# Performance work log

Hardware: AMD Instinct MI355X
Metric: run time of the kernel (lower is better)

## Reference

```python
import jax, jax.numpy as jnp
import numpy as np

D = 1024      # d_model
H = 16        # num_heads
DH = D // H   # head_dim = 64
BASE = 10000.0


def setup_inputs() -> dict:
    key = jax.random.key(0)
    ks = jax.random.split(key, 5)
    lengths = np.array([1024, 768, 896, 1024], dtype=np.int32)
    cu = np.concatenate([[0], np.cumsum(lengths)]).astype(np.int32)
    T = int(cu[-1])  # 3712 packed tokens
    x = jax.random.normal(ks[0], (T, D), dtype=jnp.float32)
    Wqkv = jax.random.normal(ks[1], (D, 3 * D), dtype=jnp.float32) / np.sqrt(D)
    bqkv = jax.random.normal(ks[2], (3 * D,), dtype=jnp.float32) * 0.02
    Wo = jax.random.normal(ks[3], (D, D), dtype=jnp.float32) / np.sqrt(D)
    bo = jax.random.normal(ks[4], (D,), dtype=jnp.float32) * 0.02
    return {"x": x, "Wqkv": Wqkv, "bqkv": bqkv, "Wo": Wo, "bo": bo,
            "cu_seqlens": jnp.asarray(cu), "max_seqlen": 1024}


def reference(x, Wqkv, bqkv, Wo, bo, cu_seqlens, max_seqlen):
    T = x.shape[0]
    B = cu_seqlens.shape[0] - 1
    S = int(max_seqlen)

    # fused qkv projection: [T, 3, H, DH]
    qkv = (x @ Wqkv + bqkv).reshape(T, 3, H, DH)
    q, k, v = qkv[:, 0], qkv[:, 1], qkv[:, 2]

    # per-token sequence id and within-sequence position (RoPE resets per seq)
    tok = jnp.arange(T)
    seq_id = jnp.searchsorted(cu_seqlens, tok, side='right') - 1  # [T]
    pos = tok - cu_seqlens[seq_id]                                # [T]

    # RoPE, non-interleaved (rotate-half over full head_dim)
    inv_freq = 1.0 / (BASE ** (jnp.arange(0, DH, 2, dtype=jnp.float32) / DH))
    ang = pos[:, None].astype(jnp.float32) * inv_freq             # [T, DH/2]
    cos = jnp.cos(ang)[:, None, :]                                # [T, 1, DH/2]
    sin = jnp.sin(ang)[:, None, :]

    def rope(t):
        t1, t2 = t[..., : DH // 2], t[..., DH // 2:]
        return jnp.concatenate([t1 * cos - t2 * sin, t2 * cos + t1 * sin], axis=-1)

    q, k = rope(q), rope(k)

    # scatter packed tokens into padded [B, S, H, DH] (varlen attention)
    qp = jnp.zeros((B, S, H, DH), x.dtype).at[seq_id, pos].set(q)
    kp = jnp.zeros((B, S, H, DH), x.dtype).at[seq_id, pos].set(k)
    vp = jnp.zeros((B, S, H, DH), x.dtype).at[seq_id, pos].set(v)
    valid = jnp.zeros((B, S), bool).at[seq_id, pos].set(True)

    scale = 1.0 / np.sqrt(DH)
    scores = jnp.einsum('bqhd,bkhd->bhqk', qp, kp) * scale        # [B,H,S,S]
    causal = jnp.tril(jnp.ones((S, S), bool))
    mask = causal[None, None] & valid[:, None, None, :]
    scores = jnp.where(mask, scores, jnp.asarray(-1e30, scores.dtype))
    attn = jax.nn.softmax(scores, axis=-1)
    op = jnp.einsum('bhqk,bkhd->bqhd', attn, vp)                  # [B,S,H,DH]

    # unpad back to packed layout, then output projection (W_o)
    out = op[seq_id, pos].reshape(T, D)
    return out @ Wo + bo
```

## Files before the change

kernel.cpp:

```cpp
#include <hip/hip_runtime.h>

typedef _Float16 f16;
typedef _Float16 f16x8 __attribute__((ext_vector_type(8)));
typedef _Float16 f16x4 __attribute__((ext_vector_type(4)));
typedef float f32x4 __attribute__((ext_vector_type(4)));

#define MFMA16(a, b, c) __builtin_amdgcn_mfma_f32_16x16x32_f16((a), (b), (c), 0, 0, 0)

typedef __attribute__((address_space(3))) void lds_void;
typedef const __attribute__((address_space(1))) void g_void;
__device__ __forceinline__ void async_copy16(void* lds, const void* g) {
    __builtin_amdgcn_global_load_lds((g_void*)g, (lds_void*)lds, 16, 0, 0);
}

__global__ void cvt_x(const float* __restrict__ in, f16* __restrict__ out, int n) {
    int i4 = (blockIdx.x * 256 + threadIdx.x) * 4;
    if (i4 >= n) return;
    float4 v = *reinterpret_cast<const float4*>(in + i4);
    f16x4 o;
    o[0] = (f16)v.x; o[1] = (f16)v.y; o[2] = (f16)v.z; o[3] = (f16)v.w;
    *reinterpret_cast<f16x4*>(out + i4) = o;
}

__global__ void wtrans(const float* __restrict__ in, f16* __restrict__ out, int K, int N) {
    __shared__ f16 tile[64][65];
    int n0 = blockIdx.x * 64, k0 = blockIdx.y * 64;
    int c = threadIdx.x & 63, rb = threadIdx.x >> 6;
#pragma unroll
    for (int it = 0; it < 16; ++it) {
        int r = rb + it * 4;
        tile[r][c] = (f16)in[(size_t)(k0 + r) * N + n0 + c];
    }
    __syncthreads();
#pragma unroll
    for (int it = 0; it < 16; ++it) {
        int rr = rb + it * 4;
        out[(size_t)(n0 + rr) * K + k0 + c] = tile[c][rr];
    }
}

#define BM 128
#define BN 128
#define BKK 32
__global__ __launch_bounds__(256) void gemm_tile(
    const f16* __restrict__ A, const f16* __restrict__ Bt,
    const float* __restrict__ bias, f16* __restrict__ Ch, float* __restrict__ Cf,
    int M, int N, int K) {
    __shared__ f16 lA[2][BM * BKK];
    __shared__ f16 lB[2][BN * BKK];
    int tid = threadIdx.x;
    int lane = tid & 63, w = tid >> 6;
    int lr = lane & 15, lg = lane >> 4;
    int wm = (w & 1) * 64, wn = (w >> 1) * 64;
    int bx = blockIdx.x, by = blockIdx.y;

    int srow = tid >> 2;
    int scol = (tid & 3) * 8;
    const f16* ga0 = A  + (size_t)min(by * BM + srow,      M - 1) * K + scol;
    const f16* ga1 = A  + (size_t)min(by * BM + 64 + srow, M - 1) * K + scol;
    const f16* gb0 = Bt + (size_t)min(bx * BN + srow,      N - 1) * K + scol;
    const f16* gb1 = Bt + (size_t)min(bx * BN + 64 + srow, N - 1) * K + scol;

    f32x4 acc[4][4] = {};
    int NT = K / BKK;

#define STAGE(curb, kt) do {                                        \
        int ko = (kt) * BKK;                                        \
        async_copy16(&lA[curb][w * 512],        ga0 + ko);          \
        async_copy16(&lA[curb][2048 + w * 512], ga1 + ko);          \
        async_copy16(&lB[curb][w * 512],        gb0 + ko);          \
        async_copy16(&lB[curb][2048 + w * 512], gb1 + ko);          \
    } while (0)

    STAGE(0, 0);
    __syncthreads();
    int cur = 0;
    for (int kt = 0; kt < NT; ++kt) {
        if (kt + 1 < NT) STAGE(cur ^ 1, kt + 1);
        f16x8 af[4], bf[4];
#pragma unroll
        for (int i = 0; i < 4; ++i) {
            af[i] = *reinterpret_cast<const f16x8*>(&lA[cur][(wm + i * 16 + lr) * BKK + lg * 8]);
            bf[i] = *reinterpret_cast<const f16x8*>(&lB[cur][(wn + i * 16 + lr) * BKK + lg * 8]);
        }
#pragma unroll
        for (int mi = 0; mi < 4; ++mi)
#pragma unroll
            for (int ni = 0; ni < 4; ++ni)
                acc[mi][ni] = MFMA16(af[mi], bf[ni], acc[mi][ni]);
        __syncthreads();
        cur ^= 1;
    }
#undef STAGE

#pragma unroll
    for (int mi = 0; mi < 4; ++mi) {
#pragma unroll
        for (int ni = 0; ni < 4; ++ni) {
            int col = bx * BN + wn + ni * 16 + lr;
            float bv = bias ? bias[col] : 0.f;
#pragma unroll
            for (int r = 0; r < 4; ++r) {
                int row = by * BM + wm + mi * 16 + 4 * lg + r;
                if (row >= M) continue;
                float v = acc[mi][ni][r] + bv;
                if (Ch) Ch[(size_t)row * N + col] = (f16)v;
                else    Cf[(size_t)row * N + col] = v;
            }
        }
    }
}

__global__ void rope_qk(const f16* __restrict__ qkv, const int* __restrict__ cu,
                        int Bn, int T, int Spad,
                        f16* __restrict__ qh2, f16* __restrict__ kh2) {
    int idx = blockIdx.x * 256 + threadIdx.x;
    if (idx >= T * 512) return;
    int i = idx & 31;
    int hh = (idx >> 5) & 15;
    int t = idx >> 9;
    int b = 0, pos = t;
    for (int q = 0; q < Bn; ++q) {
        int lo = cu[q], hi = cu[q + 1];
        if (t >= lo && t < hi) { b = q; pos = t - lo; break; }
    }
    float inv = exp2f((float)i * (-13.287712379549449f / 32.f));
    float ang = (float)pos * inv;
    float sn, cs;
    __sincosf(ang, &sn, &cs);
    size_t base = (size_t)t * 3072 + hh * 64 + i;
    float q1 = (float)qkv[base],        q2 = (float)qkv[base + 32];
    float k1 = (float)qkv[base + 1024], k2 = (float)qkv[base + 1056];
    size_t ob = ((size_t)(b * 16 + hh) * Spad + pos) * 64 + i;
    qh2[ob]      = (f16)(q1 * cs - q2 * sn);
    qh2[ob + 32] = (f16)(q2 * cs + q1 * sn);
    kh2[ob]      = (f16)(k1 * cs - k2 * sn);
    kh2[ob + 32] = (f16)(k2 * cs + k1 * sn);
}

__global__ void v_trans(const f16* __restrict__ qkv, const int* __restrict__ cu,
                        int Bn, int T, int Spad, f16* __restrict__ vt) {
    __shared__ f16 tile[64][65];
    int h = blockIdx.y;
    int t0 = blockIdx.x * 64;
    int c = threadIdx.x & 63, rb = threadIdx.x >> 6;
#pragma unroll
    for (int it = 0; it < 16; ++it) {
        int r = rb + it * 4;
        int t = t0 + r;
        f16 v = (f16)0.f;
        if (t < T) v = qkv[(size_t)t * 3072 + 2048 + h * 64 + c];
        tile[r][c] = v;
    }
    __syncthreads();
    int t = t0 + c;
    int bb = 0, pos = -1;
    if (t < T) {
        for (int q = 0; q < Bn; ++q) {
            int lo = cu[q], hi = cu[q + 1];
            if (t >= lo && t < hi) { bb = q; pos = t - lo; }
        }
    }
#pragma unroll
    for (int it = 0; it < 16; ++it) {
        int d = rb + it * 4;
        if (pos >= 0) vt[((size_t)(bb * 16 + h) * 64 + d) * Spad + pos] = tile[c][d];
    }
}

__global__ __launch_bounds__(64) void attn_fwd(
    const f16* __restrict__ qh2, const f16* __restrict__ kh2,
    const f16* __restrict__ vt, const int* __restrict__ cu,
    f16* __restrict__ oh, int Spad, int nq, int Bn) {
    int wgid = blockIdx.x;
    int nbh = Bn * 16;
    int b, h, qi;
    if ((nbh & 7) == 0) {
        int xcd = wgid & 7, rest = wgid >> 3, nbh8 = nbh >> 3;
        int bhhi = rest % nbh8;
        qi = (nq - 1) - rest / nbh8;
        int bhv = (bhhi << 3) | xcd;
        b = bhv >> 4; h = bhv & 15;
    } else {
        qi = wgid % nq;
        int bhv = wgid / nq;
        b = bhv >> 4; h = bhv & 15;
    }
    int bh = b * 16 + h;
    int s0 = cu[b];
    int len = cu[b + 1] - s0;
    int q0 = qi * 32;
    if (q0 >= len) return;
    int lane = threadIdx.x & 63, lr = lane & 15, lg = lane >> 4;
    __shared__ f16 pl[2][16][40];

    const f16* qbase = qh2 + (size_t)bh * Spad * 64;
    const f16* kbase = kh2 + (size_t)bh * Spad * 64;
    const f16* vbase = vt  + (size_t)bh * 64 * Spad;

    f16x8 qf[2][2];
#pragma unroll
    for (int qt = 0; qt < 2; ++qt) {
        const f16* qp = qbase + (size_t)(q0 + 16 * qt + lr) * 64 + 8 * lg;
        qf[qt][0] = *reinterpret_cast<const f16x8*>(qp);
        qf[qt][1] = *reinterpret_cast<const f16x8*>(qp + 32);
    }
    float mrun[2] = {-1e30f, -1e30f}, lrun[2] = {0.f, 0.f};
    f32x4 oacc[2][4] = {};

    int kend = min(q0 + 32, len);
    for (int kk0 = 0; kk0 < kend; kk0 += 32) {
        f16x8 kf[2][2];
#pragma unroll
        for (int j = 0; j < 2; ++j) {
            const f16* kp = kbase + (size_t)(kk0 + 16 * j + lr) * 64 + 8 * lg;
            kf[j][0] = *reinterpret_cast<const f16x8*>(kp);
            kf[j][1] = *reinterpret_cast<const f16x8*>(kp + 32);
        }
        f32x4 st[2][2];
#pragma unroll
        for (int qt = 0; qt < 2; ++qt)
#pragma unroll
            for (int j = 0; j < 2; ++j) {
                f32x4 z = {0, 0, 0, 0};
                z = MFMA16(kf[j][0], qf[qt][0], z);
                z = MFMA16(kf[j][1], qf[qt][1], z);
                st[qt][j] = z;
            }
#pragma unroll
        for (int qt = 0; qt < 2; ++qt) {
            int qr = q0 + 16 * qt + lr;
            float sv[2][4];
            float mx = -1e30f;
#pragma unroll
            for (int j = 0; j < 2; ++j)
#pragma unroll
                for (int r = 0; r < 4; ++r) {
                    int kc = kk0 + 16 * j + 4 * lg + r;
                    float v = st[qt][j][r] * 0.125f;
                    if (kc > qr || kc >= len) v = -1e30f;
                    sv[j][r] = v;
                    mx = fmaxf(mx, v);
                }
            mx = fmaxf(mx, __shfl_xor(mx, 16, 64));
            mx = fmaxf(mx, __shfl_xor(mx, 32, 64));
            float mnew = fmaxf(mrun[qt], mx);
            float al = __expf(mrun[qt] - mnew);
            mrun[qt] = mnew;
            float rs = 0.f;
            f16x4 pk0, pk1;
#pragma unroll
            for (int r = 0; r < 4; ++r) {
                float p0 = __expf(sv[0][r] - mnew);
                float p1 = __expf(sv[1][r] - mnew);
                rs += p0 + p1;
                pk0[r] = (f16)p0;
                pk1[r] = (f16)p1;
            }
            rs += __shfl_xor(rs, 16, 64);
            rs += __shfl_xor(rs, 32, 64);
            lrun[qt] = lrun[qt] * al + rs;
            *reinterpret_cast<f16x4*>(&pl[qt][lr][4 * lg])      = pk0;
            *reinterpret_cast<f16x4*>(&pl[qt][lr][16 + 4 * lg]) = pk1;
#pragma unroll
            for (int dt = 0; dt < 4; ++dt)
#pragma unroll
                for (int r = 0; r < 4; ++r) oacc[qt][dt][r] *= al;
        }
        __syncthreads();
        f16x8 pa0 = *reinterpret_cast<const f16x8*>(&pl[0][lr][8 * lg]);
        f16x8 pa1 = *reinterpret_cast<const f16x8*>(&pl[1][lr][8 * lg]);
#pragma unroll
        for (int dt = 0; dt < 4; ++dt) {
            f16x8 vf = *reinterpret_cast<const f16x8*>(vbase + (size_t)(16 * dt + lr) * Spad + kk0 + 8 * lg);
            oacc[0][dt] = MFMA16(vf, pa0, oacc[0][dt]);
            oacc[1][dt] = MFMA16(vf, pa1, oacc[1][dt]);
        }
        __syncthreads();
    }
#pragma unroll
    for (int qt = 0; qt < 2; ++qt) {
        int qr = q0 + 16 * qt + lr;
        if (qr >= len) continue;
        float linv = 1.f / lrun[qt];
        f16* orow = oh + (size_t)(s0 + qr) * 1024 + h * 64;
#pragma unroll
        for (int dt = 0; dt < 4; ++dt) {
            f16x4 ov;
#pragma unroll
            for (int r = 0; r < 4; ++r) ov[r] = (f16)(oacc[qt][dt][r] * linv);
            *reinterpret_cast<f16x4*>(orow + 16 * dt + 4 * lg) = ov;
        }
    }
}

extern "C" void kernel_launch(void* const* d_in, const int* in_sizes, int n_in,
                              void* d_out, int out_size, void* d_ws, size_t ws_size,
                              hipStream_t stream) {
    const float* x    = (const float*)d_in[0];
    const float* Wqkv = (const float*)d_in[1];
    const float* bqkv = (const float*)d_in[2];
    const float* Wo   = (const float*)d_in[3];
    const float* bo   = (const float*)d_in[4];
    const int*   cu   = (const int*)d_in[5];

    const int Dm = 1024;
    int T  = in_sizes[0] / Dm;
    int Bn = in_sizes[5] - 1;
    int Spad = 1024;

    auto al = [](size_t v) { return (v + 255) & ~(size_t)255; };
    char* w = (char*)d_ws;
    size_t off = 0;
    f16* xh     = (f16*)(w + off); off = al(off + (size_t)2 * T * 1024);
    f16* qkvh   = (f16*)(w + off); off = al(off + (size_t)2 * T * 3072);
    f16* wqkvT  = (f16*)(w + off); off = al(off + (size_t)2 * 3072 * 1024);
    f16* woT    = (f16*)(w + off); off = al(off + (size_t)2 * 1024 * 1024);
    f16* qh2    = (f16*)(w + off); off = al(off + (size_t)2 * Bn * 16 * 64 * (size_t)Spad);
    f16* kh2    = (f16*)(w + off); off = al(off + (size_t)2 * Bn * 16 * 64 * (size_t)Spad);
    f16* vtp    = (f16*)(w + off); off = al(off + (size_t)2 * Bn * 16 * 64 * (size_t)Spad);
    f16* ohp    = (f16*)(w + off); off = al(off + (size_t)2 * T * 1024);
    (void)ws_size;

    {
        int n = T * 1024;
        cvt_x<<<(n / 4 + 255) / 256, 256, 0, stream>>>(x, xh, n);
    }
    wtrans<<<dim3(3072 / 64, 1024 / 64), 256, 0, stream>>>(Wqkv, wqkvT, 1024, 3072);
    wtrans<<<dim3(1024 / 64, 1024 / 64), 256, 0, stream>>>(Wo, woT, 1024, 1024);
    {
        dim3 g(3072 / BN, (T + BM - 1) / BM);
        gemm_tile<<<g, 256, 0, stream>>>(xh, wqkvT, bqkv, qkvh, nullptr, T, 3072, 1024);
    }
    {
        int total = T * 512;
        rope_qk<<<(total + 255) / 256, 256, 0, stream>>>(qkvh, cu, Bn, T, Spad, qh2, kh2);
    }
    v_trans<<<dim3((T + 63) / 64, 16), 256, 0, stream>>>(qkvh, cu, Bn, T, Spad, vtp);
    {
        int nq = Spad / 32;
        int ngrid = nq * 16 * Bn;
        attn_fwd<<<ngrid, 64, 0, stream>>>(qh2, kh2, vtp, cu, ohp, Spad, nq, Bn);
    }
    {
        dim3 g(1024 / BN, (T + BM - 1) / BM);
        gemm_tile<<<g, 256, 0, stream>>>(ohp, woT, bo, nullptr, (float*)d_out, T, 1024, 1024);
    }
}
```

Before: 149.0 us.

## Widen attention query tile, prefetch K, prescale Q, remap GEMM tiles across XCDs

The attention kernel now processes 64 query rows per single-wave workgroup instead of 32, so each K/V tile loaded is reused across four 16-row query tiles. The next K tile is register-prefetched during softmax. The 1/sqrt(d) scale moves into the RoPE kernel's Q write, removing a multiply per score. The GEMM switches to a 1D grid with an XCD-aware tile remap to improve L2 locality. Costs include higher register pressure and fewer attention workgroups, plus extra causal-masked work at the diagonal with the larger tile.

```diff
diff --git a/kernel.cpp b/kernel.cpp
--- a/kernel.cpp
+++ b/kernel.cpp
@@ -45,14 +45,17 @@
 __global__ __launch_bounds__(256) void gemm_tile(
     const f16* __restrict__ A, const f16* __restrict__ Bt,
     const float* __restrict__ bias, f16* __restrict__ Ch, float* __restrict__ Cf,
-    int M, int N, int K) {
+    int M, int N, int K, int nbx) {
     __shared__ f16 lA[2][BM * BKK];
     __shared__ f16 lB[2][BN * BKK];
     int tid = threadIdx.x;
     int lane = tid & 63, w = tid >> 6;
     int lr = lane & 15, lg = lane >> 4;
     int wm = (w & 1) * 64, wn = (w >> 1) * 64;
-    int bx = blockIdx.x, by = blockIdx.y;
+
+    int nwg = gridDim.x, wg = blockIdx.x;
+    int tile = ((nwg & 7) == 0) ? ((wg & 7) * (nwg >> 3) + (wg >> 3)) : wg;
+    int by = tile / nbx, bx = tile % nbx;
 
     int srow = tid >> 2;
     int scol = (tid & 3) * 8;
@@ -132,8 +135,8 @@
     float q1 = (float)qkv[base],        q2 = (float)qkv[base + 32];
     float k1 = (float)qkv[base + 1024], k2 = (float)qkv[base + 1056];
     size_t ob = ((size_t)(b * 16 + hh) * Spad + pos) * 64 + i;
-    qh2[ob]      = (f16)(q1 * cs - q2 * sn);
-    qh2[ob + 32] = (f16)(q2 * cs + q1 * sn);
+    qh2[ob]      = (f16)((q1 * cs - q2 * sn) * 0.125f);
+    qh2[ob + 32] = (f16)((q2 * cs + q1 * sn) * 0.125f);
     kh2[ob]      = (f16)(k1 * cs - k2 * sn);
     kh2[ob + 32] = (f16)(k2 * cs + k1 * sn);
 }
@@ -189,37 +192,42 @@
     int bh = b * 16 + h;
     int s0 = cu[b];
     int len = cu[b + 1] - s0;
-    int q0 = qi * 32;
+    int q0 = qi * 64;
     if (q0 >= len) return;
     int lane = threadIdx.x & 63, lr = lane & 15, lg = lane >> 4;
-    __shared__ f16 pl[2][16][40];
+    __shared__ f16 pl[4][16][40];
 
     const f16* qbase = qh2 + (size_t)bh * Spad * 64;
     const f16* kbase = kh2 + (size_t)bh * Spad * 64;
     const f16* vbase = vt  + (size_t)bh * 64 * Spad;
 
-    f16x8 qf[2][2];
-#pragma unroll
-    for (int qt = 0; qt < 2; ++qt) {
+    f16x8 qf[4][2];
+#pragma unroll
+    for (int qt = 0; qt < 4; ++qt) {
         const f16* qp = qbase + (size_t)(q0 + 16 * qt + lr) * 64 + 8 * lg;
         qf[qt][0] = *reinterpret_cast<const f16x8*>(qp);
         qf[qt][1] = *reinterpret_cast<const f16x8*>(qp + 32);
     }
-    float mrun[2] = {-1e30f, -1e30f}, lrun[2] = {0.f, 0.f};
-    f32x4 oacc[2][4] = {};
-
-    int kend = min(q0 + 32, len);
-    for (int kk0 = 0; kk0 < kend; kk0 += 32) {
-        f16x8 kf[2][2];
-#pragma unroll
-        for (int j = 0; j < 2; ++j) {
-            const f16* kp = kbase + (size_t)(kk0 + 16 * j + lr) * 64 + 8 * lg;
-            kf[j][0] = *reinterpret_cast<const f16x8*>(kp);
-            kf[j][1] = *reinterpret_cast<const f16x8*>(kp + 32);
-        }
-        f32x4 st[2][2];
-#pragma unroll
-        for (int qt = 0; qt < 2; ++qt)
+    float mrun[4] = {-1e30f, -1e30f, -1e30f, -1e30f};
+    float lrun[4] = {0.f, 0.f, 0.f, 0.f};
+    f32x4 oacc[4][4] = {};
+
+    int kend = min(q0 + 64, len);
+    int ntk = (kend + 31) >> 5;
+
+    f16x8 kf[2][2], kn[2][2];
+#pragma unroll
+    for (int j = 0; j < 2; ++j) {
+        const f16* kp = kbase + (size_t)(16 * j + lr) * 64 + 8 * lg;
+        kf[j][0] = *reinterpret_cast<const f16x8*>(kp);
+        kf[j][1] = *reinterpret_cast<const f16x8*>(kp + 32);
+    }
+
+    for (int kt = 0; kt < ntk; ++kt) {
+        int kk0 = kt << 5;
+        f32x4 st[4][2];
+#pragma unroll
+        for (int qt = 0; qt < 4; ++qt)
 #pragma unroll
             for (int j = 0; j < 2; ++j) {
                 f32x4 z = {0, 0, 0, 0};
@@ -227,8 +235,16 @@
                 z = MFMA16(kf[j][1], qf[qt][1], z);
                 st[qt][j] = z;
             }
-#pragma unroll
-        for (int qt = 0; qt < 2; ++qt) {
+        if (kt + 1 < ntk) {
+#pragma unroll
+            for (int j = 0; j < 2; ++j) {
+                const f16* kp = kbase + (size_t)(kk0 + 32 + 16 * j + lr) * 64 + 8 * lg;
+                kn[j][0] = *reinterpret_cast<const f16x8*>(kp);
+                kn[j][1] = *reinterpret_cast<const f16x8*>(kp + 32);
+            }
+        }
+#pragma unroll
+        for (int qt = 0; qt < 4; ++qt) {
             int qr = q0 + 16 * qt + lr;
             float sv[2][4];
             float mx = -1e30f;
@@ -237,7 +253,7 @@
 #pragma unroll
                 for (int r = 0; r < 4; ++r) {
                     int kc = kk0 + 16 * j + 4 * lg + r;
-                    float v = st[qt][j][r] * 0.125f;
+                    float v = st[qt][j][r];
                     if (kc > qr || kc >= len) v = -1e30f;
                     sv[j][r] = v;
                     mx = fmaxf(mx, v);
@@ -268,18 +284,26 @@
                 for (int r = 0; r < 4; ++r) oacc[qt][dt][r] *= al;
         }
         __syncthreads();
-        f16x8 pa0 = *reinterpret_cast<const f16x8*>(&pl[0][lr][8 * lg]);
-        f16x8 pa1 = *reinterpret_cast<const f16x8*>(&pl[1][lr][8 * lg]);
+        f16x8 pa[4];
+#pragma unroll
+        for (int qt = 0; qt < 4; ++qt)
+            pa[qt] = *reinterpret_cast<const f16x8*>(&pl[qt][lr][8 * lg]);
 #pragma unroll
         for (int dt = 0; dt < 4; ++dt) {
             f16x8 vf = *reinterpret_cast<const f16x8*>(vbase + (size_t)(16 * dt + lr) * Spad + kk0 + 8 * lg);
-            oacc[0][dt] = MFMA16(vf, pa0, oacc[0][dt]);
-            oacc[1][dt] = MFMA16(vf, pa1, oacc[1][dt]);
+#pragma unroll
+            for (int qt = 0; qt < 4; ++qt)
+                oacc[qt][dt] = MFMA16(vf, pa[qt], oacc[qt][dt]);
         }
         __syncthreads();
-    }
-#pragma unroll
-    for (int qt = 0; qt < 2; ++qt) {
+#pragma unroll
+        for (int j = 0; j < 2; ++j) {
+            kf[j][0] = kn[j][0];
+            kf[j][1] = kn[j][1];
+        }
+    }
+#pragma unroll
+    for (int qt = 0; qt < 4; ++qt) {
         int qr = q0 + 16 * qt + lr;
         if (qr >= len) continue;
         float linv = 1.f / lrun[qt];
@@ -329,8 +353,8 @@
     wtrans<<<dim3(3072 / 64, 1024 / 64), 256, 0, stream>>>(Wqkv, wqkvT, 1024, 3072);
     wtrans<<<dim3(1024 / 64, 1024 / 64), 256, 0, stream>>>(Wo, woT, 1024, 1024);
     {
-        dim3 g(3072 / BN, (T + BM - 1) / BM);
-        gemm_tile<<<g, 256, 0, stream>>>(xh, wqkvT, bqkv, qkvh, nullptr, T, 3072, 1024);
+        int nbx = 3072 / BN, nby = (T + BM - 1) / BM;
+        gemm_tile<<<nbx * nby, 256, 0, stream>>>(xh, wqkvT, bqkv, qkvh, nullptr, T, 3072, 1024, nbx);
     }
     {
         int total = T * 512;
@@ -338,12 +362,12 @@
     }
     v_trans<<<dim3((T + 63) / 64, 16), 256, 0, stream>>>(qkvh, cu, Bn, T, Spad, vtp);
     {
-        int nq = Spad / 32;
+        int nq = Spad / 64;
         int ngrid = nq * 16 * Bn;
         attn_fwd<<<ngrid, 64, 0, stream>>>(qh2, kh2, vtp, cu, ohp, Spad, nq, Bn);
     }
     {
-        dim3 g(1024 / BN, (T + BM - 1) / BM);
-        gemm_tile<<<g, 256, 0, stream>>>(ohp, woT, bo, nullptr, (float*)d_out, T, 1024, 1024);
-    }
-}
+        int nbx = 1024 / BN, nby = (T + BM - 1) / BM;
+        gemm_tile<<<nbx * nby, 256, 0, stream>>>(ohp, woT, bo, nullptr, (float*)d_out, T, 1024, 1024, nbx);
+    }
+}
```

New measurement: 167.5 us. 1.12x slower.
